# Performance work log

Hardware: AMD Instinct MI355X
Metric: run time of the kernel (lower is better)

## Reference

```python
import jax, jax.numpy as jnp
import numpy as np

DIM = 768
N_HEADS = 12
HEAD_DIM = DIM // N_HEADS
SCALE = 1.0 / (DIM ** 0.5)  # NOTE: module divides by sqrt(dim), not sqrt(head_dim)


def setup_inputs() -> dict:
    key = jax.random.key(0)
    ks = jax.random.split(key, 9)
    B, N = 16, 1024
    std = 1.0 / np.sqrt(DIM)
    inputs = jax.random.normal(ks[0], (B, N, DIM), dtype=jnp.float32)
    Wq = jax.random.normal(ks[1], (DIM, DIM), dtype=jnp.float32) * std
    bq = jax.random.normal(ks[2], (DIM,), dtype=jnp.float32) * std
    Wk = jax.random.normal(ks[3], (DIM, DIM), dtype=jnp.float32) * std
    bk = jax.random.normal(ks[4], (DIM,), dtype=jnp.float32) * std
    Wv = jax.random.normal(ks[5], (DIM, DIM), dtype=jnp.float32) * std
    bv = jax.random.normal(ks[6], (DIM,), dtype=jnp.float32) * std
    Wo = jax.random.normal(ks[7], (DIM, DIM), dtype=jnp.float32) * std
    bo = jax.random.normal(ks[8], (DIM,), dtype=jnp.float32) * std
    return {"inputs": inputs, "Wq": Wq, "bq": bq, "Wk": Wk, "bk": bk,
            "Wv": Wv, "bv": bv, "Wo": Wo, "bo": bo}


def _split_heads(x, B, N):
    # [B, N, DIM] -> [B, H, N, hd]
    return x.reshape(B, N, N_HEADS, HEAD_DIM).transpose(0, 2, 1, 3)


def reference(inputs, Wq, bq, Wk, bk, Wv, bv, Wo, bo):
    B, N, _ = inputs.shape
    q = _split_heads(inputs @ Wq + bq, B, N)
    k = _split_heads(inputs @ Wk + bk, B, N)
    v = _split_heads(inputs @ Wv + bv, B, N)
    scores = jnp.einsum('bhqd,bhkd->bhqk', q, k) * SCALE
    attn = jax.nn.softmax(scores, axis=-1)
    out = jnp.einsum('bhqk,bhkd->bhqd', attn, v)
    out = out.transpose(0, 2, 1, 3).reshape(B, N, DIM)
    return out @ Wo + bo
```

## Files before the change

kernel.cpp:

```cpp
#include <hip/hip_runtime.h>
#include <hip/hip_bf16.h>
#include <math.h>

#define DIM 768
#define NH 12
#define HD 64
#define BATCH 16
#define SEQ 1024
#define M_TOTAL (BATCH * SEQ)
#define MATE ((size_t)M_TOTAL * DIM)

typedef unsigned short ushort_t;
typedef __attribute__((ext_vector_type(8))) short short8;
typedef __attribute__((ext_vector_type(4))) float floatx4;

__device__ __constant__ float kScale = 0.03608439182435161f;

__device__ inline ushort_t f2b(float x) {
    __hip_bfloat16 h = __float2bfloat16(x);
    return __builtin_bit_cast(ushort_t, h);
}
__device__ inline float b2f_u32(unsigned int bits16) {
    union { unsigned int i; float f; } c;
    c.i = bits16 << 16;
    return c.f;
}
__device__ inline float b2f(ushort_t u) { return b2f_u32((unsigned int)u); }

__device__ __forceinline__ void gl2lds16(const ushort_t* g, ushort_t* l) {
    __builtin_amdgcn_global_load_lds(
        (__attribute__((address_space(1))) void*)g,
        (__attribute__((address_space(3))) void*)l, 16, 0, 0);
}

__global__ __launch_bounds__(256) void cvt_bf16_kernel(
    const float* __restrict__ X, ushort_t* __restrict__ Y, int n4)
{
    int i = blockIdx.x * 256 + threadIdx.x;
    if (i >= n4) return;
    float4 v = ((const float4*)X)[i];
    ushort4 o;
    o.x = f2b(v.x); o.y = f2b(v.y); o.z = f2b(v.z); o.w = f2b(v.w);
    ((ushort4*)Y)[i] = o;
}

__global__ __launch_bounds__(256) void transpose4_kernel(
    const float* __restrict__ W0, const float* __restrict__ W1,
    const float* __restrict__ W2, const float* __restrict__ W3,
    ushort_t* __restrict__ qkv_t, ushort_t* __restrict__ o_t)
{
    const int z = blockIdx.z;
    const float* W = (z == 0) ? W0 : (z == 1) ? W1 : (z == 2) ? W2 : W3;
    ushort_t* hi = (z < 3) ? qkv_t + (size_t)z * DIM * DIM : o_t;

    __shared__ float t[64][65];
    const int k0 = blockIdx.x * 64, n0 = blockIdx.y * 64;
    const int lr = threadIdx.x >> 2, lc = (threadIdx.x & 3) * 16;
    #pragma unroll
    for (int j = 0; j < 4; ++j) {
        float4 v = *(const float4*)&W[(size_t)(k0 + lr) * DIM + n0 + lc + j * 4];
        t[lr][lc + j * 4 + 0] = v.x;
        t[lr][lc + j * 4 + 1] = v.y;
        t[lr][lc + j * 4 + 2] = v.z;
        t[lr][lc + j * 4 + 3] = v.w;
    }
    __syncthreads();
    #pragma unroll
    for (int j = 0; j < 16; ++j)
        hi[(size_t)(n0 + lr) * DIM + k0 + lc + j] = f2b(t[lc + j][lr]);
}

__global__ __launch_bounds__(256) void bias_concat_kernel(
    const float* __restrict__ bq, const float* __restrict__ bk,
    const float* __restrict__ bv, float* __restrict__ ball)
{
    int i = blockIdx.x * 256 + threadIdx.x;
    if (i >= 3 * DIM) return;
    float v = (i < DIM) ? bq[i] : (i < 2 * DIM ? bk[i - DIM] : bv[i - 2 * DIM]);
    ball[i] = v;
}

template <int EPI>
__global__ __launch_bounds__(256) void mfma_gemm(
    const ushort_t* __restrict__ A, const ushort_t* __restrict__ Bhi,
    const float* __restrict__ bias, void* __restrict__ Cout)
{
    __shared__ ushort_t sA[128 * 32];
    __shared__ ushort_t sB[128 * 32];

    const int bid = blockIdx.x;
    const int xcd = bid & 7;
    const int o = bid >> 3;
    const int row0 = (xcd * 16 + (o & 15)) * 128;
    const int col0 = (o >> 4) * 128;

    const int tid = threadIdx.x;
    const int lane = tid & 63;
    const int wave = tid >> 6;
    const int wm = (wave & 1) * 64;
    const int wn = (wave >> 1) * 64;
    const int m16 = lane & 15;
    const int quad = lane >> 4;

    const int srow = lane >> 2;
    const int schunk = (lane & 3) * 8;

    const size_t aoff = (size_t)(row0 + wave * 32 + srow) * DIM + schunk;
    const size_t boff = (size_t)(col0 + wave * 32 + srow) * DIM + schunk;
    ushort_t* lA0 = sA + wave * 1024;
    ushort_t* lA1 = lA0 + 512;
    ushort_t* lB0 = sB + wave * 1024;
    ushort_t* lB1 = lB0 + 512;

    floatx4 acc[4][4];
    #pragma unroll
    for (int i = 0; i < 4; ++i)
        #pragma unroll
        for (int j = 0; j < 4; ++j)
            acc[i][j] = (floatx4){0.f, 0.f, 0.f, 0.f};

    for (int k0 = 0; k0 < DIM; k0 += 32) {
        __syncthreads();
        gl2lds16(A + aoff + k0, lA0);
        gl2lds16(A + aoff + (size_t)16 * DIM + k0, lA1);
        gl2lds16(Bhi + boff + k0, lB0);
        gl2lds16(Bhi + boff + (size_t)16 * DIM + k0, lB1);
        __syncthreads();

        short8 af[4], bh[4];
        #pragma unroll
        for (int i = 0; i < 4; ++i) {
            af[i] = *(const short8*)&sA[(wm + i * 16 + m16) * 32 + quad * 8];
            bh[i] = *(const short8*)&sB[(wn + i * 16 + m16) * 32 + quad * 8];
        }
        #pragma unroll
        for (int i = 0; i < 4; ++i)
            #pragma unroll
            for (int j = 0; j < 4; ++j)
                acc[i][j] = __builtin_amdgcn_mfma_f32_16x16x32_bf16(af[i], bh[j], acc[i][j], 0, 0, 0);
    }

    if (EPI == 0) {
        const int proj = col0 / DIM;
        const int rem0 = col0 % DIM;
        const float sc = (proj == 0) ? kScale : 1.0f;
        ushort_t* C = (ushort_t*)Cout + (size_t)proj * MATE;
        #pragma unroll
        for (int j = 0; j < 4; ++j) {
            const int coff = wn + j * 16 + m16;
            const int cc = rem0 + coff;
            const int h = cc >> 6, dd = cc & 63;
            const float bs = bias[col0 + coff];
            #pragma unroll
            for (int i = 0; i < 4; ++i)
                #pragma unroll
                for (int r = 0; r < 4; ++r) {
                    const int m = row0 + wm + i * 16 + quad * 4 + r;
                    const int bb = m >> 10, nn = m & 1023;
                    if (proj < 2) {
                        C[(((size_t)(bb * NH + h) * SEQ + nn) << 6) + dd] =
                            f2b((acc[i][j][r] + bs) * sc);
                    } else {
                        C[((((size_t)(bb * NH + h) << 6) + dd) << 10) + nn] =
                            f2b(acc[i][j][r] + bs);
                    }
                }
        }
    } else {
        float* C = (float*)Cout;
        #pragma unroll
        for (int j = 0; j < 4; ++j) {
            const int coff = wn + j * 16 + m16;
            const float bs = bias[col0 + coff];
            #pragma unroll
            for (int i = 0; i < 4; ++i)
                #pragma unroll
                for (int r = 0; r < 4; ++r) {
                    const int m = row0 + wm + i * 16 + quad * 4 + r;
                    C[(size_t)m * DIM + col0 + coff] = acc[i][j][r] + bs;
                }
        }
    }
}

#define APK 72
__global__ __launch_bounds__(256) void attn_kernel(
    const ushort_t* __restrict__ Q, const ushort_t* __restrict__ K,
    const ushort_t* __restrict__ Vt, ushort_t* __restrict__ Aout)
{
    __shared__ ushort_t Ks[64 * APK];
    __shared__ ushort_t Vs[64 * APK];
    __shared__ ushort_t Ps[128 * APK];

    const int bid = blockIdx.x;
    const int xcd = bid & 7;
    const int o = bid >> 3;
    const int bh = xcd * 24 + (o >> 3);
    const int q0 = (o & 7) * 128;

    const int tid = threadIdx.x;
    const int lane = tid & 63;
    const int wave = tid >> 6;
    const int wq = wave * 32;
    const int m16 = lane & 15;
    const int quad = lane >> 4;
    const size_t base  = (size_t)bh * SEQ * HD;
    const size_t baseT = (size_t)bh * HD * SEQ;

    const int sr = tid >> 2;
    const int sc = (tid & 3) * 16;

    short8 qf[2][2];
    #pragma unroll
    for (int f = 0; f < 2; ++f)
        #pragma unroll
        for (int kc = 0; kc < 2; ++kc)
            qf[f][kc] = *(const short8*)&Q[base +
                (size_t)(q0 + wq + f * 16 + m16) * HD + kc * 32 + quad * 8];

    floatx4 oacc[2][4];
    float lacc[2][4];
    #pragma unroll
    for (int f = 0; f < 2; ++f) {
        #pragma unroll
        for (int dt = 0; dt < 4; ++dt) oacc[f][dt] = (floatx4){0.f, 0.f, 0.f, 0.f};
        #pragma unroll
        for (int r = 0; r < 4; ++r) lacc[f][r] = 0.0f;
    }

    uint4 kv0 = *(const uint4*)&K[base + (size_t)sr * HD + sc];
    uint4 kv1 = *(const uint4*)&K[base + (size_t)sr * HD + sc + 8];
    uint4 vv0 = *(const uint4*)&Vt[baseT + (size_t)sr * SEQ + sc];
    uint4 vv1 = *(const uint4*)&Vt[baseT + (size_t)sr * SEQ + sc + 8];

    for (int kt = 0; kt < SEQ / 64; ++kt) {
        __syncthreads();
        *(uint4*)&Ks[sr * APK + sc] = kv0;
        *(uint4*)&Ks[sr * APK + sc + 8] = kv1;
        *(uint4*)&Vs[sr * APK + sc] = vv0;
        *(uint4*)&Vs[sr * APK + sc + 8] = vv1;
        __syncthreads();
        if (kt + 1 < SEQ / 64) {
            const int k1 = (kt + 1) * 64;
            kv0 = *(const uint4*)&K[base + (size_t)(k1 + sr) * HD + sc];
            kv1 = *(const uint4*)&K[base + (size_t)(k1 + sr) * HD + sc + 8];
            vv0 = *(const uint4*)&Vt[baseT + (size_t)sr * SEQ + k1 + sc];
            vv1 = *(const uint4*)&Vt[baseT + (size_t)sr * SEQ + k1 + sc + 8];
        }

        short8 kf[2][4];
        #pragma unroll
        for (int kc = 0; kc < 2; ++kc)
            #pragma unroll
            for (int t = 0; t < 4; ++t)
                kf[kc][t] = *(const short8*)&Ks[(t * 16 + m16) * APK + kc * 32 + quad * 8];
        floatx4 sacc[2][4];
        #pragma unroll
        for (int f = 0; f < 2; ++f)
            #pragma unroll
            for (int t = 0; t < 4; ++t)
                sacc[f][t] = (floatx4){0.f, 0.f, 0.f, 0.f};
        #pragma unroll
        for (int kc = 0; kc < 2; ++kc)
            #pragma unroll
            for (int f = 0; f < 2; ++f)
                #pragma unroll
                for (int t = 0; t < 4; ++t)
                    sacc[f][t] = __builtin_amdgcn_mfma_f32_16x16x32_bf16(
                        qf[f][kc], kf[kc][t], sacc[f][t], 0, 0, 0);

        #pragma unroll
        for (int f = 0; f < 2; ++f)
            #pragma unroll
            for (int r = 0; r < 4; ++r) {
                float rs = 0.0f;
                #pragma unroll
                for (int t = 0; t < 4; ++t) {
                    ushort_t u = f2b(__expf(sacc[f][t][r]));
                    Ps[(wq + f * 16 + quad * 4 + r) * APK + t * 16 + m16] = u;
                    rs += b2f(u);
                }
                lacc[f][r] += rs;
            }

        short8 vf[2][4];
        #pragma unroll
        for (int kc = 0; kc < 2; ++kc)
            #pragma unroll
            for (int dt = 0; dt < 4; ++dt)
                vf[kc][dt] = *(const short8*)&Vs[(dt * 16 + m16) * APK + kc * 32 + quad * 8];
        #pragma unroll
        for (int f = 0; f < 2; ++f) {
            #pragma unroll
            for (int kc = 0; kc < 2; ++kc) {
                short8 pf = *(const short8*)&Ps[(wq + f * 16 + m16) * APK + kc * 32 + quad * 8];
                #pragma unroll
                for (int dt = 0; dt < 4; ++dt)
                    oacc[f][dt] = __builtin_amdgcn_mfma_f32_16x16x32_bf16(
                        pf, vf[kc][dt], oacc[f][dt], 0, 0, 0);
            }
        }
    }

    float inv[2][4];
    #pragma unroll
    for (int f = 0; f < 2; ++f)
        #pragma unroll
        for (int r = 0; r < 4; ++r) {
            float l = lacc[f][r];
            l += __shfl_xor(l, 1);
            l += __shfl_xor(l, 2);
            l += __shfl_xor(l, 4);
            l += __shfl_xor(l, 8);
            inv[f][r] = 1.0f / l;
        }

    #pragma unroll
    for (int f = 0; f < 2; ++f)
        #pragma unroll
        for (int dt = 0; dt < 4; ++dt)
            #pragma unroll
            for (int r = 0; r < 4; ++r)
                Ps[(wq + f * 16 + quad * 4 + r) * APK + dt * 16 + m16] =
                    f2b(oacc[f][dt][r] * inv[f][r]);
    __syncthreads();

    const int b = bh / NH, h = bh % NH;
    const int orow = tid >> 1;
    const int oc = (tid & 1) * 32;
    const size_t row = (size_t)b * SEQ + q0 + orow;
    #pragma unroll
    for (int j = 0; j < 4; ++j) {
        uint4 ov = *(const uint4*)&Ps[orow * APK + oc + j * 8];
        *(uint4*)&Aout[row * DIM + h * HD + oc + j * 8] = ov;
    }
}

extern "C" void kernel_launch(void* const* d_in, const int* in_sizes, int n_in,
                              void* d_out, int out_size, void* d_ws, size_t ws_size,
                              hipStream_t stream)
{
    const float* X  = (const float*)d_in[0];
    const float* Wq = (const float*)d_in[1];
    const float* bq = (const float*)d_in[2];
    const float* Wk = (const float*)d_in[3];
    const float* bk = (const float*)d_in[4];
    const float* Wv = (const float*)d_in[5];
    const float* bv = (const float*)d_in[6];
    const float* Wo = (const float*)d_in[7];
    const float* bo = (const float*)d_in[8];

    ushort_t* qkv  = (ushort_t*)d_ws;
    ushort_t* abuf = qkv + 3 * MATE;
    ushort_t* xbf  = abuf + MATE;
    ushort_t* wqkv_t = xbf + MATE;
    ushort_t* wo_t   = wqkv_t + (size_t)3 * DIM * DIM;
    float* ball = (float*)(wo_t + (size_t)DIM * DIM);

    cvt_bf16_kernel<<<(int)(MATE / 4 + 255) / 256, 256, 0, stream>>>(X, xbf, (int)(MATE / 4));
    transpose4_kernel<<<dim3(DIM / 64, DIM / 64, 4), 256, 0, stream>>>(
        Wq, Wk, Wv, Wo, wqkv_t, wo_t);
    bias_concat_kernel<<<(3 * DIM + 255) / 256, 256, 0, stream>>>(bq, bk, bv, ball);

    mfma_gemm<0><<<dim3(18 * 128), 256, 0, stream>>>(xbf, wqkv_t, ball, qkv);

    attn_kernel<<<dim3((SEQ / 128) * BATCH * NH), 256, 0, stream>>>(
        qkv, qkv + MATE, qkv + 2 * MATE, abuf);

    mfma_gemm<1><<<dim3(6 * 128), 256, 0, stream>>>(abuf, wo_t, bo, d_out);
}
```

Baseline: 329.0 us.

## Load K/V fragments directly from global memory, dropping LDS staging and barriers

The attention kernel no longer stages K and V tiles through shared memory with register prefetch and two barriers per iteration. Each wave now reads its MFMA operand fragments straight from global memory, relying on L2/L1 for reuse across the four waves. It also raises wave priority around the MFMA blocks with s_setprio. This removes barrier stalls and LDS traffic, but adds redundant global loads per wave and drops the software prefetch, so load latency is now exposed inside the loop.

```diff
diff --git a/kernel.cpp b/kernel.cpp
--- a/kernel.cpp
+++ b/kernel.cpp
@@ -188,8 +188,6 @@
     const ushort_t* __restrict__ Q, const ushort_t* __restrict__ K,
     const ushort_t* __restrict__ Vt, ushort_t* __restrict__ Aout)
 {
-    __shared__ ushort_t Ks[64 * APK];
-    __shared__ ushort_t Vs[64 * APK];
     __shared__ ushort_t Ps[128 * APK];
 
     const int bid = blockIdx.x;
@@ -207,9 +205,6 @@
     const size_t base  = (size_t)bh * SEQ * HD;
     const size_t baseT = (size_t)bh * HD * SEQ;
 
-    const int sr = tid >> 2;
-    const int sc = (tid & 3) * 16;
-
     short8 qf[2][2];
     #pragma unroll
     for (int f = 0; f < 2; ++f)
@@ -228,38 +223,23 @@
         for (int r = 0; r < 4; ++r) lacc[f][r] = 0.0f;
     }
 
-    uint4 kv0 = *(const uint4*)&K[base + (size_t)sr * HD + sc];
-    uint4 kv1 = *(const uint4*)&K[base + (size_t)sr * HD + sc + 8];
-    uint4 vv0 = *(const uint4*)&Vt[baseT + (size_t)sr * SEQ + sc];
-    uint4 vv1 = *(const uint4*)&Vt[baseT + (size_t)sr * SEQ + sc + 8];
-
     for (int kt = 0; kt < SEQ / 64; ++kt) {
-        __syncthreads();
-        *(uint4*)&Ks[sr * APK + sc] = kv0;
-        *(uint4*)&Ks[sr * APK + sc + 8] = kv1;
-        *(uint4*)&Vs[sr * APK + sc] = vv0;
-        *(uint4*)&Vs[sr * APK + sc + 8] = vv1;
-        __syncthreads();
-        if (kt + 1 < SEQ / 64) {
-            const int k1 = (kt + 1) * 64;
-            kv0 = *(const uint4*)&K[base + (size_t)(k1 + sr) * HD + sc];
-            kv1 = *(const uint4*)&K[base + (size_t)(k1 + sr) * HD + sc + 8];
-            vv0 = *(const uint4*)&Vt[baseT + (size_t)sr * SEQ + k1 + sc];
-            vv1 = *(const uint4*)&Vt[baseT + (size_t)sr * SEQ + k1 + sc + 8];
-        }
+        const int k1 = kt * 64;
 
         short8 kf[2][4];
         #pragma unroll
         for (int kc = 0; kc < 2; ++kc)
             #pragma unroll
             for (int t = 0; t < 4; ++t)
-                kf[kc][t] = *(const short8*)&Ks[(t * 16 + m16) * APK + kc * 32 + quad * 8];
+                kf[kc][t] = *(const short8*)&K[base +
+                    (size_t)(k1 + t * 16 + m16) * HD + kc * 32 + quad * 8];
         floatx4 sacc[2][4];
         #pragma unroll
         for (int f = 0; f < 2; ++f)
             #pragma unroll
             for (int t = 0; t < 4; ++t)
                 sacc[f][t] = (floatx4){0.f, 0.f, 0.f, 0.f};
+        __builtin_amdgcn_s_setprio(1);
         #pragma unroll
         for (int kc = 0; kc < 2; ++kc)
             #pragma unroll
@@ -268,6 +248,7 @@
                 for (int t = 0; t < 4; ++t)
                     sacc[f][t] = __builtin_amdgcn_mfma_f32_16x16x32_bf16(
                         qf[f][kc], kf[kc][t], sacc[f][t], 0, 0, 0);
+        __builtin_amdgcn_s_setprio(0);
 
         #pragma unroll
         for (int f = 0; f < 2; ++f)
@@ -288,7 +269,9 @@
         for (int kc = 0; kc < 2; ++kc)
             #pragma unroll
             for (int dt = 0; dt < 4; ++dt)
-                vf[kc][dt] = *(const short8*)&Vs[(dt * 16 + m16) * APK + kc * 32 + quad * 8];
+                vf[kc][dt] = *(const short8*)&Vt[baseT +
+                    (size_t)(dt * 16 + m16) * SEQ + k1 + kc * 32 + quad * 8];
+        __builtin_amdgcn_s_setprio(1);
         #pragma unroll
         for (int f = 0; f < 2; ++f) {
             #pragma unroll
@@ -300,6 +283,7 @@
                         pf, vf[kc][dt], oacc[f][dt], 0, 0, 0);
             }
         }
+        __builtin_amdgcn_s_setprio(0);
     }
 
     float inv[2][4];
```

After: 423.2 us. +28.6%, slower.

## Keep softmax probabilities in registers via transposed QK MFMA and lane shuffles

Applied to the files above, without the earlier changes.

The QK^T MFMA now takes its operands swapped, so each lane holds score columns that can be packed into bf16 pairs. These are redistributed with cross-lane shuffles into the A-operand layout for the PV MFMA, which removes the write and read of the Ps tile through LDS on every key tile. The softmax row sums are computed by an extra MFMA against a vector of ones instead of scalar accumulation followed by a shuffle reduction. In exchange it adds 8 shuffles per fragment plus one extra MFMA per fragment, and it increases register pressure.

```diff
diff --git a/kernel.cpp b/kernel.cpp
--- a/kernel.cpp
+++ b/kernel.cpp
@@ -210,6 +210,14 @@
     const int sr = tid >> 2;
     const int sc = (tid & 3) * 16;
 
+    const int srcA = (quad & 1) * 32 + m16;
+    const int srcB = srcA + 16;
+    const bool thi = (quad & 2) != 0;
+
+    short8 onesv;
+    #pragma unroll
+    for (int j = 0; j < 8; ++j) onesv[j] = (short)0x3F80;
+
     short8 qf[2][2];
     #pragma unroll
     for (int f = 0; f < 2; ++f)
@@ -219,13 +227,12 @@
                 (size_t)(q0 + wq + f * 16 + m16) * HD + kc * 32 + quad * 8];
 
     floatx4 oacc[2][4];
-    float lacc[2][4];
+    floatx4 lx[2];
     #pragma unroll
     for (int f = 0; f < 2; ++f) {
         #pragma unroll
         for (int dt = 0; dt < 4; ++dt) oacc[f][dt] = (floatx4){0.f, 0.f, 0.f, 0.f};
-        #pragma unroll
-        for (int r = 0; r < 4; ++r) lacc[f][r] = 0.0f;
+        lx[f] = (floatx4){0.f, 0.f, 0.f, 0.f};
     }
 
     uint4 kv0 = *(const uint4*)&K[base + (size_t)sr * HD + sc];
@@ -267,20 +274,20 @@
                 #pragma unroll
                 for (int t = 0; t < 4; ++t)
                     sacc[f][t] = __builtin_amdgcn_mfma_f32_16x16x32_bf16(
-                        qf[f][kc], kf[kc][t], sacc[f][t], 0, 0, 0);
-
+                        kf[kc][t], qf[f][kc], sacc[f][t], 0, 0, 0);
+
+        unsigned pk[2][4][2];
         #pragma unroll
         for (int f = 0; f < 2; ++f)
             #pragma unroll
-            for (int r = 0; r < 4; ++r) {
-                float rs = 0.0f;
-                #pragma unroll
-                for (int t = 0; t < 4; ++t) {
-                    ushort_t u = f2b(__expf(sacc[f][t][r]));
-                    Ps[(wq + f * 16 + quad * 4 + r) * APK + t * 16 + m16] = u;
-                    rs += b2f(u);
-                }
-                lacc[f][r] += rs;
+            for (int t = 0; t < 4; ++t) {
+                ushort2 w0, w1;
+                w0.x = f2b(__expf(sacc[f][t][0]));
+                w0.y = f2b(__expf(sacc[f][t][1]));
+                w1.x = f2b(__expf(sacc[f][t][2]));
+                w1.y = f2b(__expf(sacc[f][t][3]));
+                pk[f][t][0] = __builtin_bit_cast(unsigned, w0);
+                pk[f][t][1] = __builtin_bit_cast(unsigned, w1);
             }
 
         short8 vf[2][4];
@@ -289,31 +296,40 @@
             #pragma unroll
             for (int dt = 0; dt < 4; ++dt)
                 vf[kc][dt] = *(const short8*)&Vs[(dt * 16 + m16) * APK + kc * 32 + quad * 8];
-        #pragma unroll
-        for (int f = 0; f < 2; ++f) {
+
+        #pragma unroll
+        for (int f = 0; f < 2; ++f)
             #pragma unroll
             for (int kc = 0; kc < 2; ++kc) {
-                short8 pf = *(const short8*)&Ps[(wq + f * 16 + m16) * APK + kc * 32 + quad * 8];
+                const unsigned aA0 = (unsigned)__shfl((int)pk[f][kc * 2 + 0][0], srcA);
+                const unsigned bA0 = (unsigned)__shfl((int)pk[f][kc * 2 + 1][0], srcA);
+                const unsigned aA1 = (unsigned)__shfl((int)pk[f][kc * 2 + 0][1], srcA);
+                const unsigned bA1 = (unsigned)__shfl((int)pk[f][kc * 2 + 1][1], srcA);
+                const unsigned aB0 = (unsigned)__shfl((int)pk[f][kc * 2 + 0][0], srcB);
+                const unsigned bB0 = (unsigned)__shfl((int)pk[f][kc * 2 + 1][0], srcB);
+                const unsigned aB1 = (unsigned)__shfl((int)pk[f][kc * 2 + 0][1], srcB);
+                const unsigned bB1 = (unsigned)__shfl((int)pk[f][kc * 2 + 1][1], srcB);
+                uint4 wi;
+                wi.x = thi ? bA0 : aA0;
+                wi.y = thi ? bA1 : aA1;
+                wi.z = thi ? bB0 : aB0;
+                wi.w = thi ? bB1 : aB1;
+                const short8 pf = __builtin_bit_cast(short8, wi);
                 #pragma unroll
                 for (int dt = 0; dt < 4; ++dt)
                     oacc[f][dt] = __builtin_amdgcn_mfma_f32_16x16x32_bf16(
                         pf, vf[kc][dt], oacc[f][dt], 0, 0, 0);
+                lx[f] = __builtin_amdgcn_mfma_f32_16x16x32_bf16(
+                    pf, onesv, lx[f], 0, 0, 0);
             }
-        }
     }
 
     float inv[2][4];
     #pragma unroll
     for (int f = 0; f < 2; ++f)
         #pragma unroll
-        for (int r = 0; r < 4; ++r) {
-            float l = lacc[f][r];
-            l += __shfl_xor(l, 1);
-            l += __shfl_xor(l, 2);
-            l += __shfl_xor(l, 4);
-            l += __shfl_xor(l, 8);
-            inv[f][r] = 1.0f / l;
-        }
+        for (int r = 0; r < 4; ++r)
+            inv[f][r] = 1.0f / lx[f][r];
 
     #pragma unroll
     for (int f = 0; f < 2; ++f)
```

Result: slower. 345.5 us (+5.0%).
